# Kernel optimization log

Hardware: AMD Instinct MI355X
Metric: run time of the kernel (lower is better)

## Reference

```python
import jax, jax.numpy as jnp
import numpy as np

B, H, S, D = 4, 16, 2048, 128
NEG = -1000000000.0


def setup_inputs() -> dict:
    key = jax.random.key(0)
    kq, kk, kv, km = jax.random.split(key, 4)
    Q = jax.random.normal(kq, (B, H, S, D), dtype=jnp.float32)
    K = jax.random.normal(kk, (B, H, S, D), dtype=jnp.float32)
    V = jax.random.normal(kv, (B, H, S, D), dtype=jnp.float32)
    mask = jax.random.randint(km, (B, 1, S, S), 0, 2, dtype=jnp.int32)
    return {"Q": Q, "K": K, "V": V, "mask": mask}


def reference(Q, K, V, mask):
    # NOTE: original module computes d_k but never scales -> no 1/sqrt(d_k).
    scores = jnp.einsum("bhqd,bhkd->bhqk", Q, K)  # [B,H,S,S]
    scores = jnp.where(mask == 0, NEG, scores)
    attn = jax.nn.softmax(scores, axis=-1)
    out = jnp.einsum("bhqk,bhkd->bhqd", attn, V)  # [B,H,S,D]
    return out
```

## Files before the change

kernel.cpp:

```cpp
#include <hip/hip_runtime.h>
#include <hip/hip_bf16.h>

#define B_ 4
#define H_ 16
#define S_ 2048
#define D_ 128
#define NEGV -1000000000.0f
#define LOG2E 1.44269504f
#define THR 9.0f

typedef _Float16 f16;
typedef __attribute__((ext_vector_type(8))) _Float16 f16x8;
typedef __attribute__((ext_vector_type(4))) _Float16 f16x4v;
typedef __attribute__((ext_vector_type(2))) __fp16 fp16x2_b;
typedef __attribute__((ext_vector_type(4))) float f32x4;

__device__ inline unsigned int pack2h(float lo, float hi){
  union { f16 h[2]; unsigned int u; } cv;
  cv.h[0] = (f16)lo; cv.h[1] = (f16)hi;
  return cv.u;
}
__device__ inline unsigned short f2h16(float x){
  union { f16 h; unsigned short u; } cv; cv.h = (f16)x; return cv.u;
}
__device__ inline unsigned int pkrtz(float a, float b){
  union { fp16x2_b h; unsigned int u; } cv;
  cv.h = __builtin_amdgcn_cvt_pkrtz(a, b);
  return cv.u;
}
__device__ inline void async16(void* l, const void* g){
  __builtin_amdgcn_global_load_lds(
      (const __attribute__((address_space(1))) unsigned int*)g,
      (__attribute__((address_space(3))) unsigned int*)l, 16, 0, 0);
}

constexpr size_t MBW     = (size_t)B_*S_*(S_/32);
constexpr size_t KBYTES  = (size_t)B_*H_*S_*D_*2;
constexpr size_t WS_MID  = MBW*4 + 2*KBYTES;

__global__ __launch_bounds__(256)
void prepass(const float* __restrict__ K, const float* __restrict__ V,
             const int* __restrict__ mask, unsigned int* __restrict__ mbits,
             char* __restrict__ wsK, char* __restrict__ wsV)
{
  __shared__ char Vim[16384];
  int bid = blockIdx.x, tid = threadIdx.x;
  size_t base = (size_t)bid * (64*128);
  const float* kp = K + base;
  char* ok = wsK + (size_t)bid*16384;
  #pragma unroll
  for (int j = 0; j < 8; ++j){
    int f = tid + j*256; int kr = f>>5, c = f&31;
    float4 v = *(const float4*)(kp + kr*128 + c*4);
    unsigned int lo = pack2h(v.x, v.y), hi = pack2h(v.z, v.w);
    int off = (kr*256 + c*8) ^ ((kr&7)<<4);
    *(uint2*)(ok + off) = make_uint2(lo, hi);
  }
  const float* vp = V + base;
  #pragma unroll
  for (int j = 0; j < 8; ++j){
    int f = tid + j*256; int k = f>>5, c = f&31;
    float4 v = *(const float4*)(vp + k*128 + c*4);
    float e[4] = {v.x, v.y, v.z, v.w};
    #pragma unroll
    for (int u = 0; u < 4; ++u){
      int d = c*4 + u;
      *(unsigned short*)(Vim + d*128 + ((2*k) ^ ((d&7)<<4))) = f2h16(e[u]);
    }
  }
  __syncthreads();
  char* ov = wsV + (size_t)bid*16384;
  #pragma unroll
  for (int j = 0; j < 4; ++j)
    *(uint4*)(ov + tid*16 + j*4096) = *(const uint4*)(Vim + tid*16 + j*4096);
  {
    size_t wdx = (size_t)bid*256 + tid;
    const int* p = mask + wdx*32;
    unsigned int o = 0;
    #pragma unroll
    for (int i = 0; i < 32; i += 4){
      int4 m4 = *(const int4*)(p + i);
      o |= (m4.x ? 1u<<i : 0u) | (m4.y ? 1u<<(i+1) : 0u)
         | (m4.z ? 1u<<(i+2) : 0u) | (m4.w ? 1u<<(i+3) : 0u);
    }
    mbits[wdx] = o;
  }
}

#define ITER(KB, KC, VC, KS, VS, MWI0, MWI1, MWO0, MWO1, LAST)                 \
  do {                                                                         \
    if (!(LAST)){                                                              \
      MWO0 = mr0[(KB)+1];  MWO1 = mr1[(KB)+1];                                 \
      const char* gk_ = gK + (size_t)((KB)+1)*16384;                           \
      const char* gv_ = gV + (size_t)((KB)+1)*16384;                           \
      _Pragma("unroll")                                                        \
      for (int j = 0; j < 4; ++j){                                             \
        async16((KS) + tid*16 + j*4096, gk_ + j*4096);                         \
        async16((VS) + tid*16 + j*4096, gv_ + j*4096);                         \
      }                                                                        \
      asm volatile("s_waitcnt vmcnt(10)" ::: "memory");                        \
    } else {                                                                   \
      asm volatile("s_waitcnt vmcnt(0)" ::: "memory");                         \
    }                                                                          \
    __builtin_amdgcn_s_barrier();                                              \
    f32x4 st0[4], st1[4];                                                      \
    __builtin_amdgcn_s_setprio(1);                                             \
    _Pragma("unroll")                                                          \
    for (int t = 0; t < 4; ++t){                                               \
      const char* kr_ = (KC) + r256 + t*4096;                                  \
      f16x8 kf = *(const f16x8*)(kr_ + xq0);                                   \
      st0[t] = __builtin_amdgcn_mfma_f32_16x16x32_f16(kf, qf[0][0], z4, 0,0,0);\
      st1[t] = __builtin_amdgcn_mfma_f32_16x16x32_f16(kf, qf[1][0], z4, 0,0,0);\
      kf = *(const f16x8*)(kr_ + xq1);                                         \
      st0[t] = __builtin_amdgcn_mfma_f32_16x16x32_f16(kf, qf[0][1], st0[t],0,0,0);\
      st1[t] = __builtin_amdgcn_mfma_f32_16x16x32_f16(kf, qf[1][1], st1[t],0,0,0);\
      kf = *(const f16x8*)(kr_ + xq2);                                         \
      st0[t] = __builtin_amdgcn_mfma_f32_16x16x32_f16(kf, qf[0][2], st0[t],0,0,0);\
      st1[t] = __builtin_amdgcn_mfma_f32_16x16x32_f16(kf, qf[1][2], st1[t],0,0,0);\
      kf = *(const f16x8*)(kr_ + xq3);                                         \
      st0[t] = __builtin_amdgcn_mfma_f32_16x16x32_f16(kf, qf[0][3], st0[t],0,0,0);\
      st1[t] = __builtin_amdgcn_mfma_f32_16x16x32_f16(kf, qf[1][3], st1[t],0,0,0);\
    }                                                                          \
    __builtin_amdgcn_s_setprio(0);                                             \
                 \
    {                                                                          \
      unsigned int mlo = (unsigned int)((MWI0) >> sh4);                        \
      unsigned int mhi = (unsigned int)((MWI0) >> (sh4 + 32));                 \
      _Pragma("unroll")                                                        \
      for (int t = 0; t < 4; ++t){                                             \
        unsigned int tv = (t & 2) ? mhi : mlo;                                 \
        _Pragma("unroll")                                                      \
        for (int i = 0; i < 4; ++i)                                            \
          if (!((tv >> (((t&1)*16) + i)) & 1u)) st0[t][i] = NEGV;              \
      }                                                                        \
      mlo = (unsigned int)((MWI1) >> sh4);                                     \
      mhi = (unsigned int)((MWI1) >> (sh4 + 32));                              \
      _Pragma("unroll")                                                        \
      for (int t = 0; t < 4; ++t){                                             \
        unsigned int tv = (t & 2) ? mhi : mlo;                                 \
        _Pragma("unroll")                                                      \
        for (int i = 0; i < 4; ++i)                                            \
          if (!((tv >> (((t&1)*16) + i)) & 1u)) st1[t][i] = NEGV;              \
      }                                                                        \
    }                                                                          \
                                                           \
    float q00 = fmaxf(fmaxf(st0[0][0], st0[0][1]), fmaxf(st0[0][2], st0[0][3]));\
    float q01 = fmaxf(fmaxf(st0[1][0], st0[1][1]), fmaxf(st0[1][2], st0[1][3]));\
    float q02 = fmaxf(fmaxf(st0[2][0], st0[2][1]), fmaxf(st0[2][2], st0[2][3]));\
    float q03 = fmaxf(fmaxf(st0[3][0], st0[3][1]), fmaxf(st0[3][2], st0[3][3]));\
    float pmax0 = fmaxf(fmaxf(q00, q01), fmaxf(q02, q03));                     \
    float q10 = fmaxf(fmaxf(st1[0][0], st1[0][1]), fmaxf(st1[0][2], st1[0][3]));\
    float q11 = fmaxf(fmaxf(st1[1][0], st1[1][1]), fmaxf(st1[1][2], st1[1][3]));\
    float q12 = fmaxf(fmaxf(st1[2][0], st1[2][1]), fmaxf(st1[2][2], st1[2][3]));\
    float q13 = fmaxf(fmaxf(st1[3][0], st1[3][1]), fmaxf(st1[3][2], st1[3][3]));\
    float pmax1 = fmaxf(fmaxf(q10, q11), fmaxf(q12, q13));                     \
    pmax0 = fmaxf(pmax0, __shfl_xor(pmax0, 16));                               \
    pmax0 = fmaxf(pmax0, __shfl_xor(pmax0, 32));                               \
    pmax1 = fmaxf(pmax1, __shfl_xor(pmax1, 16));                               \
    pmax1 = fmaxf(pmax1, __shfl_xor(pmax1, 32));                               \
    bool need = (pmax0 > m0 + THR) || (pmax1 > m1 + THR);                      \
    if (__ballot(need)){                                                       \
      float n0 = fmaxf(m0, pmax0), n1 = fmaxf(m1, pmax1);                      \
      float cr0 = __builtin_amdgcn_exp2f((m0 - n0) * LOG2E);                   \
      float cr1 = __builtin_amdgcn_exp2f((m1 - n1) * LOG2E);                   \
      float cj0[4], cj1[4];                                                    \
      _Pragma("unroll")                                                        \
      for (int j = 0; j < 4; ++j){                                             \
        cj0[j] = __shfl(cr0, sh4 + j);                                         \
        cj1[j] = __shfl(cr1, sh4 + j);                                         \
      }                                                                        \
      _Pragma("unroll")                                                        \
      for (int dt = 0; dt < 8; ++dt)                                           \
        _Pragma("unroll")                                                      \
        for (int j = 0; j < 4; ++j){                                           \
          acc[0][dt][j] *= cj0[j];                                             \
          acc[1][dt][j] *= cj1[j];                                             \
        }                                                                      \
      _Pragma("unroll")                                                        \
      for (int j = 0; j < 4; ++j){                                             \
        accl[0][j] *= cj0[j];                                                  \
        accl[1][j] *= cj1[j];                                                  \
      }                                                                        \
      m0 = n0; m1 = n1;                                                        \
    }                                                                          \
    float mL0 = m0 * LOG2E, mL1 = m1 * LOG2E;                                  \
    f16x8 pf00, pf01, pf10, pf11;                                              \
    {                                                                          \
      _Pragma("unroll")                                                        \
      for (int t = 0; t < 4; ++t){                                             \
        float p0 = __builtin_amdgcn_exp2f(__builtin_fmaf(st0[t][0], LOG2E, -mL0));\
        float p1 = __builtin_amdgcn_exp2f(__builtin_fmaf(st0[t][1], LOG2E, -mL0));\
        float p2 = __builtin_amdgcn_exp2f(__builtin_fmaf(st0[t][2], LOG2E, -mL0));\
        float p3 = __builtin_amdgcn_exp2f(__builtin_fmaf(st0[t][3], LOG2E, -mL0));\
        *(uint2*)(prow + xpt[t]) = make_uint2(pkrtz(p0,p1), pkrtz(p2,p3));     \
      }                                                                        \
      pf00 = *(const f16x8*)(prow + xq0);                                      \
      pf01 = *(const f16x8*)(prow + xq1);                                      \
      _Pragma("unroll")                                                        \
      for (int t = 0; t < 4; ++t){                                             \
        float p0 = __builtin_amdgcn_exp2f(__builtin_fmaf(st1[t][0], LOG2E, -mL1));\
        float p1 = __builtin_amdgcn_exp2f(__builtin_fmaf(st1[t][1], LOG2E, -mL1));\
        float p2 = __builtin_amdgcn_exp2f(__builtin_fmaf(st1[t][2], LOG2E, -mL1));\
        float p3 = __builtin_amdgcn_exp2f(__builtin_fmaf(st1[t][3], LOG2E, -mL1));\
        *(uint2*)(prow + xpt[t]) = make_uint2(pkrtz(p0,p1), pkrtz(p2,p3));     \
      }                                                                        \
      pf10 = *(const f16x8*)(prow + xq0);                                      \
      pf11 = *(const f16x8*)(prow + xq1);                                      \
    }                                                                          \
    accl[0] = __builtin_amdgcn_mfma_f32_16x16x32_f16(pf00, ones, accl[0], 0,0,0);\
    accl[0] = __builtin_amdgcn_mfma_f32_16x16x32_f16(pf01, ones, accl[0], 0,0,0);\
    accl[1] = __builtin_amdgcn_mfma_f32_16x16x32_f16(pf10, ones, accl[1], 0,0,0);\
    accl[1] = __builtin_amdgcn_mfma_f32_16x16x32_f16(pf11, ones, accl[1], 0,0,0);\
    __builtin_amdgcn_s_setprio(1);                                             \
    _Pragma("unroll")                                                          \
    for (int dt = 0; dt < 8; ++dt){                                            \
      const char* vr_ = (VC) + r128 + dt*2048;                                 \
      f16x8 v0 = *(const f16x8*)(vr_ + xq0);                                   \
      f16x8 v1 = *(const f16x8*)(vr_ + xq1);                                   \
      acc[0][dt] = __builtin_amdgcn_mfma_f32_16x16x32_f16(pf00, v0, acc[0][dt], 0,0,0);\
      acc[0][dt] = __builtin_amdgcn_mfma_f32_16x16x32_f16(pf01, v1, acc[0][dt], 0,0,0);\
      acc[1][dt] = __builtin_amdgcn_mfma_f32_16x16x32_f16(pf10, v0, acc[1][dt], 0,0,0);\
      acc[1][dt] = __builtin_amdgcn_mfma_f32_16x16x32_f16(pf11, v1, acc[1][dt], 0,0,0);\
    }                                                                          \
    __builtin_amdgcn_s_setprio(0);                                             \
    __builtin_amdgcn_s_barrier();                                              \
  } while(0)

__global__ __launch_bounds__(256, 2)
void attn_fast(const float* __restrict__ Q,
               const unsigned long long* __restrict__ mbits,
               const char* __restrict__ wsK, const char* __restrict__ wsV,
               float* __restrict__ out)
{
  __shared__ char KB0[16384];
  __shared__ char KB1[16384];
  __shared__ char VB0[16384];
  __shared__ char VB1[16384];
  __shared__ char PL[8192];

  int bid = blockIdx.x;
  int wg = (bid & 7) * 128 + (bid >> 3);
  int bh = wg >> 4, qb = wg & 15;
  int b  = bh >> 4;
  int tid = threadIdx.x;
  int w = tid >> 6, lane = tid & 63;
  int g = lane >> 4, r = lane & 15;
  int sw = (r & 7) << 4;
  int sh4 = g * 4;
  size_t base = (size_t)bh * (S_*D_);
  int qg0 = qb*128 + w*32 + r;
  int qg1 = qg0 + 16;
  char* prow = PL + (w*16 + r)*128;

  int r256 = r*256, r128 = r*128;
  int xq0 = (g*16) ^ sw;
  int xq1 = (64 + g*16) ^ sw;
  int xq2 = (128 + g*16) ^ sw;
  int xq3 = (192 + g*16) ^ sw;
  int xpt[4];
  #pragma unroll
  for (int t = 0; t < 4; ++t) xpt[t] = (t*32 + g*8) ^ sw;

  f16x8 qf[2][4];
  #pragma unroll
  for (int u = 0; u < 2; ++u){
    const float* qp = Q + base + (size_t)(u ? qg1 : qg0) * D_;
    #pragma unroll
    for (int dc = 0; dc < 4; ++dc){
      float4 a = *(const float4*)(qp + dc*32 + g*8);
      float4 c = *(const float4*)(qp + dc*32 + g*8 + 4);
      f16x8 q8;
      q8[0]=(f16)a.x; q8[1]=(f16)a.y; q8[2]=(f16)a.z; q8[3]=(f16)a.w;
      q8[4]=(f16)c.x; q8[5]=(f16)c.y; q8[6]=(f16)c.z; q8[7]=(f16)c.w;
      qf[u][dc] = q8;
    }
  }

  const char* gK = wsK + (size_t)(bh*32)*16384 + tid*16;
  const char* gV = wsV + (size_t)(bh*32)*16384 + tid*16;
  const unsigned long long* mr0 = mbits + ((size_t)b*S_ + qg0)*32;
  const unsigned long long* mr1 = mbits + ((size_t)b*S_ + qg1)*32;

  unsigned long long mwA0 = mr0[0], mwA1 = mr1[0];
  unsigned long long mwB0 = 0, mwB1 = 0;
  #pragma unroll
  for (int j = 0; j < 4; ++j){
    async16(KB0 + tid*16 + j*4096, gK + j*4096);
    async16(VB0 + tid*16 + j*4096, gV + j*4096);
  }

  float m0 = -3.0e38f, m1 = -3.0e38f;
  f32x4 acc[2][8];
  f32x4 accl[2];
  f32x4 z4 = (f32x4){0.f,0.f,0.f,0.f};
  #pragma unroll
  for (int u = 0; u < 2; ++u){
    accl[u] = z4;
    #pragma unroll
    for (int i = 0; i < 8; ++i) acc[u][i] = z4;
  }
  f16x8 ones;
  #pragma unroll
  for (int i = 0; i < 8; ++i) ones[i] = (f16)1.0f;

  for (int kb2 = 0; kb2 < 32; kb2 += 2){
    ITER(kb2,   KB0, VB0, KB1, VB1, mwA0, mwA1, mwB0, mwB1, false);
    ITER(kb2+1, KB1, VB1, KB0, VB0, mwB0, mwB1, mwA0, mwA1, (kb2 == 30));
  }

  #pragma unroll
  for (int u = 0; u < 2; ++u){
    float inv[4];
    #pragma unroll
    for (int j = 0; j < 4; ++j) inv[j] = 1.f / accl[u][j];
    size_t ob = base + (size_t)(qb*128 + w*32 + u*16) * D_;
    #pragma unroll
    for (int dt = 0; dt < 8; ++dt){
      int d = dt*16 + r;
      #pragma unroll
      for (int j = 0; j < 4; ++j)
        out[ob + (size_t)(sh4 + j)*D_ + d] = acc[u][dt][j] * inv[j];
    }
  }
}

constexpr int VTS = 68;
constexpr int PSS = 72;

__global__ __launch_bounds__(256)
void attn_fwd(const float* __restrict__ Q, const float* __restrict__ K,
              const float* __restrict__ V, const int* __restrict__ mask,
              float* __restrict__ out)
{
  __shared__ unsigned short Klds[64 * D_];
  __shared__ unsigned short Vt[D_ * VTS];
  __shared__ unsigned short Plds[4 * 16 * PSS];

  int bid = blockIdx.x;
  int wg = (bid & 7) * 256 + (bid >> 3);
  int bh = wg >> 5, qb = wg & 31;
  int b  = bh >> 4;
  int tid = threadIdx.x;
  int w = tid >> 6, lane = tid & 63;
  int g = lane >> 4, r = lane & 15;
  size_t base = (size_t)bh * S_ * D_;
  int qg = qb * 64 + w * 16 + r;

  f16x8 qf[4];
  {
    const float* qp = Q + base + (size_t)qg * D_;
    #pragma unroll
    for (int dc = 0; dc < 4; ++dc){
      float4 a = *reinterpret_cast<const float4*>(qp + dc*32 + g*8);
      float4 c = *reinterpret_cast<const float4*>(qp + dc*32 + g*8 + 4);
      f16x8 q8;
      q8[0]=(f16)a.x; q8[1]=(f16)a.y; q8[2]=(f16)a.z; q8[3]=(f16)a.w;
      q8[4]=(f16)c.x; q8[5]=(f16)c.y; q8[6]=(f16)c.z; q8[7]=(f16)c.w;
      qf[dc] = q8;
    }
  }

  float mrun = -3.0e38f, lrun = 0.f;
  f32x4 acc[8];
  #pragma unroll
  for (int i = 0; i < 8; ++i) acc[i] = (f32x4){0.f,0.f,0.f,0.f};

  for (int kb = 0; kb < S_/64; ++kb){
    const float* kp = K + base + (size_t)(kb*64) * D_;
    #pragma unroll
    for (int i = 0; i < 8; ++i){
      int f = tid + i*256;
      int kr = f >> 5, c = f & 31;
      float4 v = *reinterpret_cast<const float4*>(kp + kr*D_ + c*4);
      unsigned int lo = pack2h(v.x, v.y), hi = pack2h(v.z, v.w);
      int off = (kr*256 + c*8) ^ ((kr & 7) << 4);
      *reinterpret_cast<uint2*>(reinterpret_cast<char*>(Klds) + off) = make_uint2(lo, hi);
    }
    const float* vp = V + base + (size_t)(kb*64) * D_;
    #pragma unroll
    for (int i = 0; i < 4; ++i){
      int f = tid + i*256;
      int p = f >> 5, c = f & 31;
      float4 v0 = *reinterpret_cast<const float4*>(vp + (size_t)(2*p)*D_ + c*4);
      float4 v1 = *reinterpret_cast<const float4*>(vp + (size_t)(2*p+1)*D_ + c*4);
      float e0[4] = {v0.x, v0.y, v0.z, v0.w};
      float e1[4] = {v1.x, v1.y, v1.z, v1.w};
      #pragma unroll
      for (int j = 0; j < 4; ++j){
        int d = c*4 + j;
        *reinterpret_cast<unsigned int*>(reinterpret_cast<char*>(Vt) + (d*VTS + 2*p)*2)
            = pack2h(e0[j], e1[j]);
      }
    }
    __syncthreads();

    f32x4 st[4];
    #pragma unroll
    for (int t = 0; t < 4; ++t){
      f32x4 s = (f32x4){0.f,0.f,0.f,0.f};
      int row = t*16 + r;
      #pragma unroll
      for (int dc = 0; dc < 4; ++dc){
        int off = row*256 + ((dc*64 + g*16) ^ ((row & 7) << 4));
        f16x8 kf = *reinterpret_cast<const f16x8*>(reinterpret_cast<const char*>(Klds) + off);
        s = __builtin_amdgcn_mfma_f32_16x16x32_f16(kf, qf[dc], s, 0, 0, 0);
      }
      st[t] = s;
    }

    #pragma unroll
    for (int t = 0; t < 4; ++t){
      int4 m4 = *reinterpret_cast<const int4*>(
          mask + ((size_t)b * S_ + qg) * S_ + kb*64 + t*16 + g*4);
      if (!m4.x) st[t][0] = NEGV;
      if (!m4.y) st[t][1] = NEGV;
      if (!m4.z) st[t][2] = NEGV;
      if (!m4.w) st[t][3] = NEGV;
    }

    float pmax = st[0][0];
    #pragma unroll
    for (int t = 0; t < 4; ++t)
      #pragma unroll
      for (int i = 0; i < 4; ++i) pmax = fmaxf(pmax, st[t][i]);
    pmax = fmaxf(pmax, __shfl_xor(pmax, 16));
    pmax = fmaxf(pmax, __shfl_xor(pmax, 32));
    float mnew = fmaxf(mrun, pmax);
    float corr = __builtin_amdgcn_exp2f((mrun - mnew) * LOG2E);
    float psum = 0.f;
    char* prow = reinterpret_cast<char*>(Plds) + (size_t)(w*16 + r)*PSS*2;
    #pragma unroll
    for (int t = 0; t < 4; ++t){
      float p0 = __builtin_amdgcn_exp2f((st[t][0]-mnew)*LOG2E);
      float p1 = __builtin_amdgcn_exp2f((st[t][1]-mnew)*LOG2E);
      float p2 = __builtin_amdgcn_exp2f((st[t][2]-mnew)*LOG2E);
      float p3 = __builtin_amdgcn_exp2f((st[t][3]-mnew)*LOG2E);
      psum += (p0+p1)+(p2+p3);
      char* pb = prow + (t*16 + g*4)*2;
      *reinterpret_cast<unsigned int*>(pb)     = pack2h(p0, p1);
      *reinterpret_cast<unsigned int*>(pb + 4) = pack2h(p2, p3);
    }
    psum += __shfl_xor(psum, 16);
    psum += __shfl_xor(psum, 32);
    lrun = lrun * corr + psum;
    mrun = mnew;
    float cq0 = __shfl(corr, g*4 + 0);
    float cq1 = __shfl(corr, g*4 + 1);
    float cq2 = __shfl(corr, g*4 + 2);
    float cq3 = __shfl(corr, g*4 + 3);
    #pragma unroll
    for (int dt = 0; dt < 8; ++dt){
      acc[dt][0] *= cq0; acc[dt][1] *= cq1; acc[dt][2] *= cq2; acc[dt][3] *= cq3;
    }

    f16x8 pf0 = *reinterpret_cast<const f16x8*>(prow + g*16);
    f16x8 pf1 = *reinterpret_cast<const f16x8*>(prow + 64 + g*16);
    #pragma unroll
    for (int dt = 0; dt < 8; ++dt){
      int vo = (dt*16 + r)*VTS*2 + g*16;
      const char* vb = reinterpret_cast<const char*>(Vt);
      union { f16x8 v; f16x4v h[2]; } uv0, uv1;
      uv0.h[0] = *reinterpret_cast<const f16x4v*>(vb + vo);
      uv0.h[1] = *reinterpret_cast<const f16x4v*>(vb + vo + 8);
      acc[dt] = __builtin_amdgcn_mfma_f32_16x16x32_f16(pf0, uv0.v, acc[dt], 0, 0, 0);
      uv1.h[0] = *reinterpret_cast<const f16x4v*>(vb + vo + 64);
      uv1.h[1] = *reinterpret_cast<const f16x4v*>(vb + vo + 72);
      acc[dt] = __builtin_amdgcn_mfma_f32_16x16x32_f16(pf1, uv1.v, acc[dt], 0, 0, 0);
    }
    __syncthreads();
  }

  float l0 = __shfl(lrun, g*4 + 0);
  float l1 = __shfl(lrun, g*4 + 1);
  float l2 = __shfl(lrun, g*4 + 2);
  float l3 = __shfl(lrun, g*4 + 3);
  float i0 = 1.f/l0, i1 = 1.f/l1, i2 = 1.f/l2, i3 = 1.f/l3;
  size_t obase = base + (size_t)(qb*64 + w*16) * D_;
  #pragma unroll
  for (int dt = 0; dt < 8; ++dt){
    int d = dt*16 + r;
    out[obase + (size_t)(g*4 + 0)*D_ + d] = acc[dt][0]*i0;
    out[obase + (size_t)(g*4 + 1)*D_ + d] = acc[dt][1]*i1;
    out[obase + (size_t)(g*4 + 2)*D_ + d] = acc[dt][2]*i2;
    out[obase + (size_t)(g*4 + 3)*D_ + d] = acc[dt][3]*i3;
  }
}

extern "C" void kernel_launch(void* const* d_in, const int* in_sizes, int n_in,
                              void* d_out, int out_size, void* d_ws, size_t ws_size,
                              hipStream_t stream) {
  const float* Q = (const float*)d_in[0];
  const float* K = (const float*)d_in[1];
  const float* V = (const float*)d_in[2];
  const int* mask = (const int*)d_in[3];
  float* out = (float*)d_out;
  dim3 blk(256);

  if (ws_size >= WS_MID){
    unsigned int* mbits = (unsigned int*)d_ws;
    char* wsK = (char*)d_ws + MBW*4;
    char* wsV = wsK + KBYTES;
    prepass<<<dim3(2048), blk, 0, stream>>>(K, V, mask, mbits, wsK, wsV);
    attn_fast<<<dim3(1024), blk, 0, stream>>>(Q, (const unsigned long long*)d_ws,
                                              wsK, wsV, out);
  } else {
    attn_fwd<<<dim3(2048), blk, 0, stream>>>(Q, K, V, mask, out);
  }
}
```

Measured before the change: 247.7 us.

## Switch attention inner loop to 32x32x16 MFMA with register-resident P

Rewrites the main attention loop to use 32x32x16 f16 MFMAs with transposed score layout so each lane owns one query row. The P matrix now moves between lanes with cross-half shuffles instead of a round trip through an LDS staging buffer, and the row sum is computed with VALU adds instead of an MFMA against ones. Output is written as contiguous float4 per row. Accumulators grow to 64 registers per lane, so launch bounds drop to one block per SIMD group, which may reduce occupancy and latency hiding.

```diff
diff --git a/kernel.cpp b/kernel.cpp
--- a/kernel.cpp
+++ b/kernel.cpp
@@ -14,6 +14,7 @@
 typedef __attribute__((ext_vector_type(4))) _Float16 f16x4v;
 typedef __attribute__((ext_vector_type(2))) __fp16 fp16x2_b;
 typedef __attribute__((ext_vector_type(4))) float f32x4;
+typedef __attribute__((ext_vector_type(16))) float f32x16;
 
 __device__ inline unsigned int pack2h(float lo, float hi){
   union { f16 h[2]; unsigned int u; } cv;
@@ -87,10 +88,12 @@
   }
 }
 
-#define ITER(KB, KC, VC, KS, VS, MWI0, MWI1, MWO0, MWO1, LAST)                 \
+union U8 { unsigned int u[4]; f16x8 v; };
+
+#define ITER(KB, KC, VC, KS, VS, MWI, MWO, LAST)                               \
   do {                                                                         \
     if (!(LAST)){                                                              \
-      MWO0 = mr0[(KB)+1];  MWO1 = mr1[(KB)+1];                                 \
+      MWO = mr[(KB)+1];                                                        \
       const char* gk_ = gK + (size_t)((KB)+1)*16384;                           \
       const char* gv_ = gV + (size_t)((KB)+1)*16384;                           \
       _Pragma("unroll")                                                        \
@@ -98,135 +101,114 @@
         async16((KS) + tid*16 + j*4096, gk_ + j*4096);                         \
         async16((VS) + tid*16 + j*4096, gv_ + j*4096);                         \
       }                                                                        \
-      asm volatile("s_waitcnt vmcnt(10)" ::: "memory");                        \
+      asm volatile("s_waitcnt vmcnt(9)" ::: "memory");                         \
     } else {                                                                   \
       asm volatile("s_waitcnt vmcnt(0)" ::: "memory");                         \
     }                                                                          \
     __builtin_amdgcn_s_barrier();                                              \
-    f32x4 st0[4], st1[4];                                                      \
+    f32x16 st0, st1;                                                           \
     __builtin_amdgcn_s_setprio(1);                                             \
     _Pragma("unroll")                                                          \
-    for (int t = 0; t < 4; ++t){                                               \
-      const char* kr_ = (KC) + r256 + t*4096;                                  \
-      f16x8 kf = *(const f16x8*)(kr_ + xq0);                                   \
-      st0[t] = __builtin_amdgcn_mfma_f32_16x16x32_f16(kf, qf[0][0], z4, 0,0,0);\
-      st1[t] = __builtin_amdgcn_mfma_f32_16x16x32_f16(kf, qf[1][0], z4, 0,0,0);\
-      kf = *(const f16x8*)(kr_ + xq1);                                         \
-      st0[t] = __builtin_amdgcn_mfma_f32_16x16x32_f16(kf, qf[0][1], st0[t],0,0,0);\
-      st1[t] = __builtin_amdgcn_mfma_f32_16x16x32_f16(kf, qf[1][1], st1[t],0,0,0);\
-      kf = *(const f16x8*)(kr_ + xq2);                                         \
-      st0[t] = __builtin_amdgcn_mfma_f32_16x16x32_f16(kf, qf[0][2], st0[t],0,0,0);\
-      st1[t] = __builtin_amdgcn_mfma_f32_16x16x32_f16(kf, qf[1][2], st1[t],0,0,0);\
-      kf = *(const f16x8*)(kr_ + xq3);                                         \
-      st0[t] = __builtin_amdgcn_mfma_f32_16x16x32_f16(kf, qf[0][3], st0[t],0,0,0);\
-      st1[t] = __builtin_amdgcn_mfma_f32_16x16x32_f16(kf, qf[1][3], st1[t],0,0,0);\
+    for (int c = 0; c < 8; ++c){                                               \
+      f16x8 kf0 = *(const f16x8*)((KC) + lo5*256 + ((c*32 + hi16) ^ swk));     \
+      f16x8 kf1 = *(const f16x8*)((KC) + (32+lo5)*256 + ((c*32 + hi16) ^ swk));\
+      st0 = __builtin_amdgcn_mfma_f32_32x32x16_f16(kf0, qfB[c],                \
+              c==0 ? z16 : st0, 0, 0, 0);                                      \
+      st1 = __builtin_amdgcn_mfma_f32_32x32x16_f16(kf1, qfB[c],                \
+              c==0 ? z16 : st1, 0, 0, 0);                                      \
     }                                                                          \
     __builtin_amdgcn_s_setprio(0);                                             \
-                 \
+            \
     {                                                                          \
-      unsigned int mlo = (unsigned int)((MWI0) >> sh4);                        \
-      unsigned int mhi = (unsigned int)((MWI0) >> (sh4 + 32));                 \
+      unsigned int mt0 = ((unsigned int)(MWI)) >> hi4;                         \
+      unsigned int mt1 = ((unsigned int)((MWI) >> 32)) >> hi4;                 \
       _Pragma("unroll")                                                        \
-      for (int t = 0; t < 4; ++t){                                             \
-        unsigned int tv = (t & 2) ? mhi : mlo;                                 \
+      for (int e = 0; e < 16; ++e){                                            \
+        int bit = 8*(e>>2) + (e&3);                                            \
+        if (!((mt0 >> bit) & 1u)) st0[e] = NEGV;                               \
+        if (!((mt1 >> bit) & 1u)) st1[e] = NEGV;                               \
+      }                                                                        \
+    }                                                                          \
+                                        \
+    float m00 = fmaxf(fmaxf(st0[0],st0[1]), fmaxf(st0[2],st0[3]));             \
+    float m01 = fmaxf(fmaxf(st0[4],st0[5]), fmaxf(st0[6],st0[7]));             \
+    float m02 = fmaxf(fmaxf(st0[8],st0[9]), fmaxf(st0[10],st0[11]));           \
+    float m03 = fmaxf(fmaxf(st0[12],st0[13]), fmaxf(st0[14],st0[15]));         \
+    float m10 = fmaxf(fmaxf(st1[0],st1[1]), fmaxf(st1[2],st1[3]));             \
+    float m11 = fmaxf(fmaxf(st1[4],st1[5]), fmaxf(st1[6],st1[7]));             \
+    float m12 = fmaxf(fmaxf(st1[8],st1[9]), fmaxf(st1[10],st1[11]));           \
+    float m13 = fmaxf(fmaxf(st1[12],st1[13]), fmaxf(st1[14],st1[15]));         \
+    float pmax = fmaxf(fmaxf(fmaxf(m00,m01), fmaxf(m02,m03)),                  \
+                       fmaxf(fmaxf(m10,m11), fmaxf(m12,m13)));                 \
+    pmax = fmaxf(pmax, __shfl_xor(pmax, 32));                                  \
+    bool need = pmax > mrun + THR;                                             \
+    if (__ballot(need)){                                                       \
+      float n = fmaxf(mrun, pmax);                                             \
+      float corr = __builtin_amdgcn_exp2f((mrun - n) * LOG2E);                 \
+      _Pragma("unroll")                                                        \
+      for (int f = 0; f < 4; ++f)                                              \
         _Pragma("unroll")                                                      \
-        for (int i = 0; i < 4; ++i)                                            \
-          if (!((tv >> (((t&1)*16) + i)) & 1u)) st0[t][i] = NEGV;              \
-      }                                                                        \
-      mlo = (unsigned int)((MWI1) >> sh4);                                     \
-      mhi = (unsigned int)((MWI1) >> (sh4 + 32));                              \
-      _Pragma("unroll")                                                        \
-      for (int t = 0; t < 4; ++t){                                             \
-        unsigned int tv = (t & 2) ? mhi : mlo;                                 \
-        _Pragma("unroll")                                                      \
-        for (int i = 0; i < 4; ++i)                                            \
-          if (!((tv >> (((t&1)*16) + i)) & 1u)) st1[t][i] = NEGV;              \
-      }                                                                        \
-    }                                                                          \
+        for (int e = 0; e < 16; ++e) acc[f][e] *= corr;                        \
+      lsum *= corr;                                                            \
+      mrun = n;                                                                \
+    }                                                                          \
+    float mL = mrun * LOG2E;                                                   \
                                                            \
-    float q00 = fmaxf(fmaxf(st0[0][0], st0[0][1]), fmaxf(st0[0][2], st0[0][3]));\
-    float q01 = fmaxf(fmaxf(st0[1][0], st0[1][1]), fmaxf(st0[1][2], st0[1][3]));\
-    float q02 = fmaxf(fmaxf(st0[2][0], st0[2][1]), fmaxf(st0[2][2], st0[2][3]));\
-    float q03 = fmaxf(fmaxf(st0[3][0], st0[3][1]), fmaxf(st0[3][2], st0[3][3]));\
-    float pmax0 = fmaxf(fmaxf(q00, q01), fmaxf(q02, q03));                     \
-    float q10 = fmaxf(fmaxf(st1[0][0], st1[0][1]), fmaxf(st1[0][2], st1[0][3]));\
-    float q11 = fmaxf(fmaxf(st1[1][0], st1[1][1]), fmaxf(st1[1][2], st1[1][3]));\
-    float q12 = fmaxf(fmaxf(st1[2][0], st1[2][1]), fmaxf(st1[2][2], st1[2][3]));\
-    float q13 = fmaxf(fmaxf(st1[3][0], st1[3][1]), fmaxf(st1[3][2], st1[3][3]));\
-    float pmax1 = fmaxf(fmaxf(q10, q11), fmaxf(q12, q13));                     \
-    pmax0 = fmaxf(pmax0, __shfl_xor(pmax0, 16));                               \
-    pmax0 = fmaxf(pmax0, __shfl_xor(pmax0, 32));                               \
-    pmax1 = fmaxf(pmax1, __shfl_xor(pmax1, 16));                               \
-    pmax1 = fmaxf(pmax1, __shfl_xor(pmax1, 32));                               \
-    bool need = (pmax0 > m0 + THR) || (pmax1 > m1 + THR);                      \
-    if (__ballot(need)){                                                       \
-      float n0 = fmaxf(m0, pmax0), n1 = fmaxf(m1, pmax1);                      \
-      float cr0 = __builtin_amdgcn_exp2f((m0 - n0) * LOG2E);                   \
-      float cr1 = __builtin_amdgcn_exp2f((m1 - n1) * LOG2E);                   \
-      float cj0[4], cj1[4];                                                    \
-      _Pragma("unroll")                                                        \
-      for (int j = 0; j < 4; ++j){                                             \
-        cj0[j] = __shfl(cr0, sh4 + j);                                         \
-        cj1[j] = __shfl(cr1, sh4 + j);                                         \
-      }                                                                        \
-      _Pragma("unroll")                                                        \
-      for (int dt = 0; dt < 8; ++dt)                                           \
-        _Pragma("unroll")                                                      \
-        for (int j = 0; j < 4; ++j){                                           \
-          acc[0][dt][j] *= cj0[j];                                             \
-          acc[1][dt][j] *= cj1[j];                                             \
-        }                                                                      \
-      _Pragma("unroll")                                                        \
-      for (int j = 0; j < 4; ++j){                                             \
-        accl[0][j] *= cj0[j];                                                  \
-        accl[1][j] *= cj1[j];                                                  \
-      }                                                                        \
-      m0 = n0; m1 = n1;                                                        \
-    }                                                                          \
-    float mL0 = m0 * LOG2E, mL1 = m1 * LOG2E;                                  \
-    f16x8 pf00, pf01, pf10, pf11;                                              \
-    {                                                                          \
-      _Pragma("unroll")                                                        \
-      for (int t = 0; t < 4; ++t){                                             \
-        float p0 = __builtin_amdgcn_exp2f(__builtin_fmaf(st0[t][0], LOG2E, -mL0));\
-        float p1 = __builtin_amdgcn_exp2f(__builtin_fmaf(st0[t][1], LOG2E, -mL0));\
-        float p2 = __builtin_amdgcn_exp2f(__builtin_fmaf(st0[t][2], LOG2E, -mL0));\
-        float p3 = __builtin_amdgcn_exp2f(__builtin_fmaf(st0[t][3], LOG2E, -mL0));\
-        *(uint2*)(prow + xpt[t]) = make_uint2(pkrtz(p0,p1), pkrtz(p2,p3));     \
-      }                                                                        \
-      pf00 = *(const f16x8*)(prow + xq0);                                      \
-      pf01 = *(const f16x8*)(prow + xq1);                                      \
-      _Pragma("unroll")                                                        \
-      for (int t = 0; t < 4; ++t){                                             \
-        float p0 = __builtin_amdgcn_exp2f(__builtin_fmaf(st1[t][0], LOG2E, -mL1));\
-        float p1 = __builtin_amdgcn_exp2f(__builtin_fmaf(st1[t][1], LOG2E, -mL1));\
-        float p2 = __builtin_amdgcn_exp2f(__builtin_fmaf(st1[t][2], LOG2E, -mL1));\
-        float p3 = __builtin_amdgcn_exp2f(__builtin_fmaf(st1[t][3], LOG2E, -mL1));\
-        *(uint2*)(prow + xpt[t]) = make_uint2(pkrtz(p0,p1), pkrtz(p2,p3));     \
-      }                                                                        \
-      pf10 = *(const f16x8*)(prow + xq0);                                      \
-      pf11 = *(const f16x8*)(prow + xq1);                                      \
-    }                                                                          \
-    accl[0] = __builtin_amdgcn_mfma_f32_16x16x32_f16(pf00, ones, accl[0], 0,0,0);\
-    accl[0] = __builtin_amdgcn_mfma_f32_16x16x32_f16(pf01, ones, accl[0], 0,0,0);\
-    accl[1] = __builtin_amdgcn_mfma_f32_16x16x32_f16(pf10, ones, accl[1], 0,0,0);\
-    accl[1] = __builtin_amdgcn_mfma_f32_16x16x32_f16(pf11, ones, accl[1], 0,0,0);\
+    float p0[16], p1[16];                                                      \
+    _Pragma("unroll")                                                          \
+    for (int e = 0; e < 16; ++e){                                              \
+      p0[e] = __builtin_amdgcn_exp2f(__builtin_fmaf(st0[e], LOG2E, -mL));      \
+      p1[e] = __builtin_amdgcn_exp2f(__builtin_fmaf(st1[e], LOG2E, -mL));      \
+    }                                                                          \
+    float s0 = ((p0[0]+p0[1])+(p0[2]+p0[3])) + ((p0[4]+p0[5])+(p0[6]+p0[7]));  \
+    float s1 = ((p0[8]+p0[9])+(p0[10]+p0[11])) + ((p0[12]+p0[13])+(p0[14]+p0[15]));\
+    float s2 = ((p1[0]+p1[1])+(p1[2]+p1[3])) + ((p1[4]+p1[5])+(p1[6]+p1[7]));  \
+    float s3 = ((p1[8]+p1[9])+(p1[10]+p1[11])) + ((p1[12]+p1[13])+(p1[14]+p1[15]));\
+    float psum = (s0+s1)+(s2+s3);                                              \
+    psum += __shfl_xor(psum, 32);                                              \
+    lsum += psum;                                                              \
+                              \
+    unsigned int u0[8], u1[8], x0[8], x1[8];                                   \
+    _Pragma("unroll")                                                          \
+    for (int gg = 0; gg < 4; ++gg){                                            \
+      u0[gg*2]   = pkrtz(p0[gg*4],   p0[gg*4+1]);                              \
+      u0[gg*2+1] = pkrtz(p0[gg*4+2], p0[gg*4+3]);                              \
+      u1[gg*2]   = pkrtz(p1[gg*4],   p1[gg*4+1]);                              \
+      u1[gg*2+1] = pkrtz(p1[gg*4+2], p1[gg*4+3]);                              \
+    }                                                                          \
+    _Pragma("unroll")                                                          \
+    for (int i = 0; i < 8; ++i){                                               \
+      x0[i] = (unsigned int)__shfl_xor((int)u0[i], 32);                        \
+      x1[i] = (unsigned int)__shfl_xor((int)u1[i], 32);                        \
+    }                                                                          \
+    U8 pb0, pb1, pb2, pb3;                                                     \
+    pb0.u[0] = hi ? x0[2] : u0[0];  pb0.u[1] = hi ? x0[3] : u0[1];             \
+    pb0.u[2] = hi ? u0[2] : x0[0];  pb0.u[3] = hi ? u0[3] : x0[1];             \
+    pb1.u[0] = hi ? x0[6] : u0[4];  pb1.u[1] = hi ? x0[7] : u0[5];             \
+    pb1.u[2] = hi ? u0[6] : x0[4];  pb1.u[3] = hi ? u0[7] : x0[5];             \
+    pb2.u[0] = hi ? x1[2] : u1[0];  pb2.u[1] = hi ? x1[3] : u1[1];             \
+    pb2.u[2] = hi ? u1[2] : x1[0];  pb2.u[3] = hi ? u1[3] : x1[1];             \
+    pb3.u[0] = hi ? x1[6] : u1[4];  pb3.u[1] = hi ? x1[7] : u1[5];             \
+    pb3.u[2] = hi ? u1[6] : x1[4];  pb3.u[3] = hi ? u1[7] : x1[5];             \
+                      \
     __builtin_amdgcn_s_setprio(1);                                             \
     _Pragma("unroll")                                                          \
-    for (int dt = 0; dt < 8; ++dt){                                            \
-      const char* vr_ = (VC) + r128 + dt*2048;                                 \
-      f16x8 v0 = *(const f16x8*)(vr_ + xq0);                                   \
-      f16x8 v1 = *(const f16x8*)(vr_ + xq1);                                   \
-      acc[0][dt] = __builtin_amdgcn_mfma_f32_16x16x32_f16(pf00, v0, acc[0][dt], 0,0,0);\
-      acc[0][dt] = __builtin_amdgcn_mfma_f32_16x16x32_f16(pf01, v1, acc[0][dt], 0,0,0);\
-      acc[1][dt] = __builtin_amdgcn_mfma_f32_16x16x32_f16(pf10, v0, acc[1][dt], 0,0,0);\
-      acc[1][dt] = __builtin_amdgcn_mfma_f32_16x16x32_f16(pf11, v1, acc[1][dt], 0,0,0);\
+    for (int f = 0; f < 4; ++f){                                               \
+      const char* vr = (VC) + (f*32 + lo5)*128;                                \
+      f16x8 va = *(const f16x8*)(vr + ((0*32 + hi16) ^ swk));                  \
+      acc[f] = __builtin_amdgcn_mfma_f32_32x32x16_f16(va, pb0.v, acc[f],0,0,0);\
+      va = *(const f16x8*)(vr + ((1*32 + hi16) ^ swk));                        \
+      acc[f] = __builtin_amdgcn_mfma_f32_32x32x16_f16(va, pb1.v, acc[f],0,0,0);\
+      va = *(const f16x8*)(vr + ((2*32 + hi16) ^ swk));                        \
+      acc[f] = __builtin_amdgcn_mfma_f32_32x32x16_f16(va, pb2.v, acc[f],0,0,0);\
+      va = *(const f16x8*)(vr + ((3*32 + hi16) ^ swk));                        \
+      acc[f] = __builtin_amdgcn_mfma_f32_32x32x16_f16(va, pb3.v, acc[f],0,0,0);\
     }                                                                          \
     __builtin_amdgcn_s_setprio(0);                                             \
     __builtin_amdgcn_s_barrier();                                              \
   } while(0)
 
-__global__ __launch_bounds__(256, 2)
+__global__ __launch_bounds__(256, 1)
 void attn_fast(const float* __restrict__ Q,
                const unsigned long long* __restrict__ mbits,
                const char* __restrict__ wsK, const char* __restrict__ wsV,
@@ -236,7 +218,6 @@
   __shared__ char KB1[16384];
   __shared__ char VB0[16384];
   __shared__ char VB1[16384];
-  __shared__ char PL[8192];
 
   int bid = blockIdx.x;
   int wg = (bid & 7) * 128 + (bid >> 3);
@@ -244,82 +225,62 @@
   int b  = bh >> 4;
   int tid = threadIdx.x;
   int w = tid >> 6, lane = tid & 63;
-  int g = lane >> 4, r = lane & 15;
-  int sw = (r & 7) << 4;
-  int sh4 = g * 4;
+  int lo5 = lane & 31, hi = lane >> 5;
+  int hi4 = hi * 4, hi16 = hi * 16;
+  int swk = (lo5 & 7) << 4;
   size_t base = (size_t)bh * (S_*D_);
-  int qg0 = qb*128 + w*32 + r;
-  int qg1 = qg0 + 16;
-  char* prow = PL + (w*16 + r)*128;
-
-  int r256 = r*256, r128 = r*128;
-  int xq0 = (g*16) ^ sw;
-  int xq1 = (64 + g*16) ^ sw;
-  int xq2 = (128 + g*16) ^ sw;
-  int xq3 = (192 + g*16) ^ sw;
-  int xpt[4];
-  #pragma unroll
-  for (int t = 0; t < 4; ++t) xpt[t] = (t*32 + g*8) ^ sw;
-
-  f16x8 qf[2][4];
-  #pragma unroll
-  for (int u = 0; u < 2; ++u){
-    const float* qp = Q + base + (size_t)(u ? qg1 : qg0) * D_;
-    #pragma unroll
-    for (int dc = 0; dc < 4; ++dc){
-      float4 a = *(const float4*)(qp + dc*32 + g*8);
-      float4 c = *(const float4*)(qp + dc*32 + g*8 + 4);
+  int qg = qb*128 + w*32 + lo5;
+
+  f16x8 qfB[8];
+  {
+    const float* qp = Q + base + (size_t)qg * D_;
+    #pragma unroll
+    for (int c = 0; c < 8; ++c){
+      float4 a = *(const float4*)(qp + c*16 + hi*8);
+      float4 d = *(const float4*)(qp + c*16 + hi*8 + 4);
       f16x8 q8;
       q8[0]=(f16)a.x; q8[1]=(f16)a.y; q8[2]=(f16)a.z; q8[3]=(f16)a.w;
-      q8[4]=(f16)c.x; q8[5]=(f16)c.y; q8[6]=(f16)c.z; q8[7]=(f16)c.w;
-      qf[u][dc] = q8;
+      q8[4]=(f16)d.x; q8[5]=(f16)d.y; q8[6]=(f16)d.z; q8[7]=(f16)d.w;
+      qfB[c] = q8;
     }
   }
 
   const char* gK = wsK + (size_t)(bh*32)*16384 + tid*16;
   const char* gV = wsV + (size_t)(bh*32)*16384 + tid*16;
-  const unsigned long long* mr0 = mbits + ((size_t)b*S_ + qg0)*32;
-  const unsigned long long* mr1 = mbits + ((size_t)b*S_ + qg1)*32;
-
-  unsigned long long mwA0 = mr0[0], mwA1 = mr1[0];
-  unsigned long long mwB0 = 0, mwB1 = 0;
+  const unsigned long long* mr = mbits + ((size_t)b*S_ + qg)*32;
+
+  unsigned long long mwA = mr[0];
+  unsigned long long mwB = 0;
   #pragma unroll
   for (int j = 0; j < 4; ++j){
     async16(KB0 + tid*16 + j*4096, gK + j*4096);
     async16(VB0 + tid*16 + j*4096, gV + j*4096);
   }
 
-  float m0 = -3.0e38f, m1 = -3.0e38f;
-  f32x4 acc[2][8];
-  f32x4 accl[2];
-  f32x4 z4 = (f32x4){0.f,0.f,0.f,0.f};
-  #pragma unroll
-  for (int u = 0; u < 2; ++u){
-    accl[u] = z4;
-    #pragma unroll
-    for (int i = 0; i < 8; ++i) acc[u][i] = z4;
-  }
-  f16x8 ones;
-  #pragma unroll
-  for (int i = 0; i < 8; ++i) ones[i] = (f16)1.0f;
+  float mrun = -3.0e38f, lsum = 0.f;
+  f32x16 acc[4];
+  f32x16 z16;
+  #pragma unroll
+  for (int e = 0; e < 16; ++e) z16[e] = 0.f;
+  #pragma unroll
+  for (int f = 0; f < 4; ++f) acc[f] = z16;
 
   for (int kb2 = 0; kb2 < 32; kb2 += 2){
-    ITER(kb2,   KB0, VB0, KB1, VB1, mwA0, mwA1, mwB0, mwB1, false);
-    ITER(kb2+1, KB1, VB1, KB0, VB0, mwB0, mwB1, mwA0, mwA1, (kb2 == 30));
-  }
-
-  #pragma unroll
-  for (int u = 0; u < 2; ++u){
-    float inv[4];
-    #pragma unroll
-    for (int j = 0; j < 4; ++j) inv[j] = 1.f / accl[u][j];
-    size_t ob = base + (size_t)(qb*128 + w*32 + u*16) * D_;
-    #pragma unroll
-    for (int dt = 0; dt < 8; ++dt){
-      int d = dt*16 + r;
-      #pragma unroll
-      for (int j = 0; j < 4; ++j)
-        out[ob + (size_t)(sh4 + j)*D_ + d] = acc[u][dt][j] * inv[j];
+    ITER(kb2,   KB0, VB0, KB1, VB1, mwA, mwB, false);
+    ITER(kb2+1, KB1, VB1, KB0, VB0, mwB, mwA, (kb2 == 30));
+  }
+
+  float inv = 1.f / lsum;
+  float* orow = out + base + (size_t)qg * D_;
+  #pragma unroll
+  for (int f = 0; f < 4; ++f){
+    #pragma unroll
+    for (int gg = 0; gg < 4; ++gg){
+      int d = f*32 + hi4 + gg*8;
+      float4 o;
+      o.x = acc[f][gg*4+0]*inv; o.y = acc[f][gg*4+1]*inv;
+      o.z = acc[f][gg*4+2]*inv; o.w = acc[f][gg*4+3]*inv;
+      *(float4*)(orow + d) = o;
     }
   }
 }
```

Result: slower. 348.7 us (+40.8%).
